# Performance work log

Hardware: AMD Instinct MI355X
Metric: run time of the kernel (lower is better)

The kernel has to match this reference:

```python
import jax, jax.numpy as jnp
import numpy as np

D_MODEL = 1024
N_HEADS = 16


def setup_inputs() -> dict:
    key0 = jax.random.key(0)
    ks = jax.random.split(key0, 13)
    B, Lq, Lk, D = 2, 1024, 2048, D_MODEL
    scale = 0.02
    inp = {
        "query": jax.random.normal(ks[0], (B, Lq, D), jnp.float32),
        "key": jax.random.normal(ks[1], (B, Lk, D), jnp.float32),
        "value": jax.random.normal(ks[2], (B, Lk, D), jnp.float32),
        "mask": jax.random.randint(ks[3], (B, 1, Lq, Lk), 0, 2, jnp.int32),
        "attn_bias": jax.random.normal(ks[4], (B, N_HEADS, Lq, Lk), jnp.float32) * 0.1,
        "Wq": jax.random.normal(ks[5], (D, D), jnp.float32) * scale,
        "bq": jnp.zeros((D,), jnp.float32),
        "Wk": jax.random.normal(ks[6], (D, D), jnp.float32) * scale,
        "bk": jnp.zeros((D,), jnp.float32),
        "Wv": jax.random.normal(ks[7], (D, D), jnp.float32) * scale,
        "bv": jnp.zeros((D,), jnp.float32),
        "Wo": jax.random.normal(ks[8], (D, D), jnp.float32) * scale,
        "bo": jnp.zeros((D,), jnp.float32),
    }
    return inp


def reference(query, key, value, mask, attn_bias, Wq, bq, Wk, bk, Wv, bv, Wo, bo):
    B, Lq, D = query.shape
    Lk = key.shape[1]
    H = N_HEADS
    dh = D // H
    # projections (torch Linear: x @ W.T + b), then split heads -> [B,H,L,dh]
    Q = (query @ Wq.T + bq).reshape(B, Lq, H, dh).transpose(0, 2, 1, 3)
    K = (key @ Wk.T + bk).reshape(B, Lk, H, dh).transpose(0, 2, 1, 3)
    V = (value @ Wv.T + bv).reshape(B, Lk, H, dh).transpose(0, 2, 1, 3)
    scores = jnp.einsum("bhqd,bhkd->bhqk", Q, K) / jnp.sqrt(jnp.float32(dh))
    scores = scores + attn_bias
    scores = jnp.where(mask == 0, jnp.float32(-1e9), scores)
    attn = jax.nn.softmax(scores, axis=-1)  # dropout disabled (eval / p=0)
    out = jnp.einsum("bhqk,bhkd->bhqd", attn, V)
    out = out.transpose(0, 2, 1, 3).reshape(B, Lq, D)
    out = out @ Wo.T + bo
    return out, attn
```

## Files before the change

kernel.cpp:

```cpp
#include <hip/hip_runtime.h>
#include <hip/hip_bf16.h>

typedef __hip_bfloat16 bf16;
typedef __bf16  bf16x8 __attribute__((ext_vector_type(8)));
typedef float   f32x4  __attribute__((ext_vector_type(4)));

static constexpr int DMODEL = 1024;
static constexpr int NHEADS = 16;
static constexpr int DHEAD  = 64;
static constexpr int BATCH  = 2;
static constexpr int SLQ    = 1024;
static constexpr int SLK    = 2048;
static constexpr size_t OUTQ = (size_t)BATCH * SLQ * DMODEL;

__device__ __forceinline__ void stage8(unsigned short* dst, const bf16* src) {
    *(int4*)dst = *(const int4*)src;
}
__device__ __forceinline__ void stage8(unsigned short* dst, const float* src) {
    const float4 a = *(const float4*)(src);
    const float4 b = *(const float4*)(src + 4);
    bf16 h[8];
    h[0] = __float2bfloat16(a.x); h[1] = __float2bfloat16(a.y);
    h[2] = __float2bfloat16(a.z); h[3] = __float2bfloat16(a.w);
    h[4] = __float2bfloat16(b.x); h[5] = __float2bfloat16(b.y);
    h[6] = __float2bfloat16(b.z); h[7] = __float2bfloat16(b.w);
    *(int4*)dst = *(const int4*)h;
}

__device__ __forceinline__ void store_one(bf16* p, float v) { *p = __float2bfloat16(v); }
__device__ __forceinline__ void store_one(float* p, float v) { *p = v; }

template <typename TA, typename TB>
__device__ __forceinline__ void gemm_core(const TA* __restrict__ At, int lda,
                                          const TB* __restrict__ Bt, int ldb,
                                          int K, f32x4 acc[2][2])
{
    __shared__ __align__(16) unsigned short As[64][40];
    __shared__ __align__(16) unsigned short Bs[64][40];
    const int tid  = threadIdx.x;
    const int lane = tid & 63;
    const int wave = tid >> 6;
    const int wr   = (wave >> 1) * 32;
    const int wc   = (wave & 1) * 32;
    const int lrow = lane & 15;
    const int koff = (lane >> 4) * 8;
    const int srow   = tid >> 2;
    const int schunk = (tid & 3) * 8;

    for (int kt = 0; kt < K; kt += 32) {
        stage8(&As[srow][schunk], At + (size_t)srow * lda + kt + schunk);
        stage8(&Bs[srow][schunk], Bt + (size_t)srow * ldb + kt + schunk);
        __syncthreads();
        bf16x8 a0 = *(const bf16x8*)(&As[wr      + lrow][koff]);
        bf16x8 a1 = *(const bf16x8*)(&As[wr + 16 + lrow][koff]);
        bf16x8 b0 = *(const bf16x8*)(&Bs[wc      + lrow][koff]);
        bf16x8 b1 = *(const bf16x8*)(&Bs[wc + 16 + lrow][koff]);
        acc[0][0] = __builtin_amdgcn_mfma_f32_16x16x32_bf16(a0, b0, acc[0][0], 0, 0, 0);
        acc[0][1] = __builtin_amdgcn_mfma_f32_16x16x32_bf16(a0, b1, acc[0][1], 0, 0, 0);
        acc[1][0] = __builtin_amdgcn_mfma_f32_16x16x32_bf16(a1, b0, acc[1][0], 0, 0, 0);
        acc[1][1] = __builtin_amdgcn_mfma_f32_16x16x32_bf16(a1, b1, acc[1][1], 0, 0, 0);
        __syncthreads();
    }
}

template <typename TA, typename TC>
__global__ __launch_bounds__(256)
void k_proj(const TA* __restrict__ A, const float* __restrict__ W,
            const float* __restrict__ bias, TC* __restrict__ C, int K, int N)
{
    const int m0 = blockIdx.x * 64;
    const int n0 = blockIdx.y * 64;
    f32x4 z = {0.f, 0.f, 0.f, 0.f};
    f32x4 acc[2][2] = {{z, z}, {z, z}};
    gemm_core(A + (size_t)m0 * K, K, W + (size_t)n0 * K, K, K, acc);
    const int lane = threadIdx.x & 63;
    const int wave = threadIdx.x >> 6;
    const int wr = (wave >> 1) * 32, wc = (wave & 1) * 32;
#pragma unroll
    for (int i = 0; i < 2; ++i)
#pragma unroll
        for (int j = 0; j < 2; ++j) {
            const int col = n0 + wc + j * 16 + (lane & 15);
            const float bv = bias[col];
#pragma unroll
            for (int r = 0; r < 4; ++r) {
                const int row = m0 + wr + i * 16 + (lane >> 4) * 4 + r;
                store_one(&C[(size_t)row * N + col], acc[i][j][r] + bv);
            }
        }
}

__global__ __launch_bounds__(256)
void k_projV(const float* __restrict__ A, const float* __restrict__ W,
             const float* __restrict__ bias, bf16* __restrict__ Vt)
{
    const int m0 = blockIdx.x * 64;
    const int n0 = blockIdx.y * 64;
    f32x4 z = {0.f, 0.f, 0.f, 0.f};
    f32x4 acc[2][2] = {{z, z}, {z, z}};
    gemm_core(A + (size_t)m0 * DMODEL, DMODEL, W + (size_t)n0 * DMODEL, DMODEL, DMODEL, acc);
    const int lane = threadIdx.x & 63;
    const int wave = threadIdx.x >> 6;
    const int wr = (wave >> 1) * 32, wc = (wave & 1) * 32;
#pragma unroll
    for (int i = 0; i < 2; ++i)
#pragma unroll
        for (int j = 0; j < 2; ++j) {
            const int col = n0 + wc + j * 16 + (lane & 15);
            const float bv = bias[col];
            const int h = col >> 6, d = col & 63;
            const int mb = m0 + wr + i * 16 + (lane >> 4) * 4;
            const int b = mb >> 11;
            const int kk = mb & 2047;
            bf16* dst = Vt + ((size_t)(b * NHEADS + h) * DHEAD + d) * SLK + kk;
#pragma unroll
            for (int r = 0; r < 4; ++r)
                dst[r] = __float2bfloat16(acc[i][j][r] + bv);
        }
}

__global__ __launch_bounds__(1024, 4)
void k_attn(const bf16* __restrict__ Qp, const bf16* __restrict__ Kp,
            const float* __restrict__ bias, const int* __restrict__ mask,
            const bf16* __restrict__ Vt, float* __restrict__ attn,
            bf16* __restrict__ ctx)
{
    constexpr int SST = 2052;
    constexpr int PST = 520;

    __shared__ __align__(16) float S[16 * SST];
    __shared__ __align__(16) bf16  Pc[16 * PST];
    __shared__ float m_s[16], inv_s[16];

    const int qt = blockIdx.x, bh = blockIdx.y;
    const int b = bh >> 4, h = bh & 15;
    const int q0 = qt * 16;
    const int tid  = threadIdx.x;
    const int lane = tid & 63, w = tid >> 6;
    const int lr = lane & 15, lk = lane >> 4;

    const bf16* qb = Qp + ((size_t)(b * SLQ + q0 + lr)) * DMODEL + h * DHEAD + lk * 8;
    const bf16x8 a0 = *(const bf16x8*)qb;
    const bf16x8 a1 = *(const bf16x8*)(qb + 32);

    const bf16* kb = Kp + (size_t)b * SLK * DMODEL + h * DHEAD + lk * 8;
#pragma unroll 2
    for (int ct = 0; ct < 8; ++ct) {
        const int c0 = w * 128 + ct * 16;
        const bf16* kp = kb + (size_t)(c0 + lr) * DMODEL;
        bf16x8 b0 = *(const bf16x8*)kp;
        bf16x8 b1 = *(const bf16x8*)(kp + 32);
        f32x4 acc = {0.f, 0.f, 0.f, 0.f};
        acc = __builtin_amdgcn_mfma_f32_16x16x32_bf16(a0, b0, acc, 0, 0, 0);
        acc = __builtin_amdgcn_mfma_f32_16x16x32_bf16(a1, b1, acc, 0, 0, 0);
#pragma unroll
        for (int r = 0; r < 4; ++r)
            S[(lk * 4 + r) * SST + c0 + lr] = acc[r] * 0.125f;
    }
    __syncthreads();

    {
        float* sp = &S[w * SST];
        const size_t brow = ((size_t)bh * SLQ + q0 + w) * SLK;
        const size_t mrow = ((size_t)b  * SLQ + q0 + w) * SLK;
        float mx = -3.0e38f;
#pragma unroll 2
        for (int j = 0; j < 8; ++j) {
            const int col = j * 256 + lane * 4;
            f32x4 v = *(const f32x4*)(sp + col);
            const float4 bb = *(const float4*)(bias + brow + col);
            const int4  mm = *(const int4*)(mask + mrow + col);
            float s0 = (mm.x == 0) ? -1e9f : v[0] + bb.x;
            float s1 = (mm.y == 0) ? -1e9f : v[1] + bb.y;
            float s2 = (mm.z == 0) ? -1e9f : v[2] + bb.z;
            float s3 = (mm.w == 0) ? -1e9f : v[3] + bb.w;
            f32x4 wv = {s0, s1, s2, s3};
            *(f32x4*)(sp + col) = wv;
            mx = fmaxf(mx, fmaxf(fmaxf(s0, s1), fmaxf(s2, s3)));
        }
#pragma unroll
        for (int d = 1; d < 64; d <<= 1) mx = fmaxf(mx, __shfl_xor(mx, d));
        float l = 0.f;
#pragma unroll 2
        for (int j = 0; j < 8; ++j) {
            const int col = j * 256 + lane * 4;
            const f32x4 v = *(const f32x4*)(sp + col);
            l += __expf(v[0] - mx) + __expf(v[1] - mx)
               + __expf(v[2] - mx) + __expf(v[3] - mx);
        }
#pragma unroll
        for (int d = 1; d < 64; d <<= 1) l += __shfl_xor(l, d);
        if (lane == 0) { m_s[w] = mx; inv_s[w] = 1.0f / l; }
    }
    __syncthreads();

    f32x4 pv = {0.f, 0.f, 0.f, 0.f};
    const int g = w >> 2, dg = w & 3;
    const bf16* vb = Vt + (size_t)bh * DHEAD * SLK + (size_t)(dg * 16 + lr) * SLK + lk * 8;
    for (int c = 0; c < 4; ++c) {
        const int ck0 = c * 512;
        {
            const int scol = lane * 8;
            const float m = m_s[w], inv = inv_s[w];
            const f32x4 s0 = *(const f32x4*)&S[w * SST + ck0 + scol];
            const f32x4 s1 = *(const f32x4*)&S[w * SST + ck0 + scol + 4];
            const f32x4 p0 = {__expf(s0[0] - m) * inv, __expf(s0[1] - m) * inv,
                              __expf(s0[2] - m) * inv, __expf(s0[3] - m) * inv};
            const f32x4 p1 = {__expf(s1[0] - m) * inv, __expf(s1[1] - m) * inv,
                              __expf(s1[2] - m) * inv, __expf(s1[3] - m) * inv};
            float* ap = attn + ((size_t)bh * SLQ + q0 + w) * SLK + ck0 + scol;
            __builtin_nontemporal_store(p0, (f32x4*)ap);
            __builtin_nontemporal_store(p1, (f32x4*)(ap + 4));
            bf16 t8[8] = {__float2bfloat16(p0[0]), __float2bfloat16(p0[1]),
                          __float2bfloat16(p0[2]), __float2bfloat16(p0[3]),
                          __float2bfloat16(p1[0]), __float2bfloat16(p1[1]),
                          __float2bfloat16(p1[2]), __float2bfloat16(p1[3])};
            *(int4*)&Pc[w * PST + scol] = *(const int4*)t8;
        }
        __syncthreads();
        const bf16* vc = vb + ck0;
#pragma unroll
        for (int i = 0; i < 4; ++i) {
            const int koff = (g * 4 + i) * 32;
            bf16x8 pa = *(const bf16x8*)&Pc[lr * PST + koff + lk * 8];
            bf16x8 vv = *(const bf16x8*)(vc + koff);
            pv = __builtin_amdgcn_mfma_f32_16x16x32_bf16(pa, vv, pv, 0, 0, 0);
        }
        __syncthreads();
    }

    float* rbuf = S;
    *(f32x4*)&rbuf[(w * 64 + lane) * 4] = pv;
    __syncthreads();
    if (g == 0) {
        f32x4 t = {0.f, 0.f, 0.f, 0.f};
#pragma unroll
        for (int gg = 0; gg < 4; ++gg)
            t += *(const f32x4*)&rbuf[((gg * 4 + dg) * 64 + lane) * 4];
        const int d = dg * 16 + lr;
#pragma unroll
        for (int r = 0; r < 4; ++r) {
            const int q = lk * 4 + r;
            ctx[((size_t)(b * SLQ + q0 + q)) * DMODEL + h * DHEAD + d] =
                __float2bfloat16(t[r]);
        }
    }
}

extern "C" void kernel_launch(void* const* d_in, const int* in_sizes, int n_in,
                              void* d_out, int out_size, void* d_ws, size_t ws_size,
                              hipStream_t stream)
{
    const float* query = (const float*)d_in[0];
    const float* key   = (const float*)d_in[1];
    const float* value = (const float*)d_in[2];
    const int*   mask  = (const int*)d_in[3];
    const float* bias  = (const float*)d_in[4];
    const float* Wq = (const float*)d_in[5];
    const float* bq = (const float*)d_in[6];
    const float* Wk = (const float*)d_in[7];
    const float* bk = (const float*)d_in[8];
    const float* Wv = (const float*)d_in[9];
    const float* bv = (const float*)d_in[10];
    const float* Wo = (const float*)d_in[11];
    const float* bo = (const float*)d_in[12];

    float* out  = (float*)d_out;
    float* attn = out + OUTQ;

    bf16* Qp  = (bf16*)d_ws;
    bf16* ctx = (bf16*)d_ws;
    bf16* Kp  = (bf16*)d_out;
    bf16* Vt  = (bf16*)d_ws + (size_t)4 * 1024 * 1024;

    dim3 blk(256);

    k_proj<float, bf16><<<dim3(BATCH * SLQ / 64, DMODEL / 64), blk, 0, stream>>>(query, Wq, bq, Qp, DMODEL, DMODEL);
    k_proj<float, bf16><<<dim3(BATCH * SLK / 64, DMODEL / 64), blk, 0, stream>>>(key,   Wk, bk, Kp, DMODEL, DMODEL);
    k_projV<<<dim3(BATCH * SLK / 64, DMODEL / 64), blk, 0, stream>>>(value, Wv, bv, Vt);
    k_attn<<<dim3(SLQ / 16, BATCH * NHEADS), dim3(1024), 0, stream>>>(Qp, Kp, bias, mask, Vt, attn, ctx);
    k_proj<bf16, float><<<dim3(BATCH * SLQ / 64, DMODEL / 64), blk, 0, stream>>>(ctx, Wo, bo, out, DMODEL, DMODEL);
}
```

Baseline: 740.4 us.

## Pre-convert inputs to bf16, fuse QKV projections into one 128x128-tile GEMM launch

Adds a single conversion kernel that casts the activations and weights to bf16 into scratch space inside the attn output buffer. Q/K/V projections are merged into one launch with 128x128 tiles and 4x4 MFMA per wave, and the output projection uses the same larger tile. This is meant to raise arithmetic intensity and stop converting fp32 inside the GEMM inner loop, at the cost of an extra full-memory pass for conversion and fewer blocks per launch.

```diff
diff --git a/kernel.cpp b/kernel.cpp
--- a/kernel.cpp
+++ b/kernel.cpp
@@ -13,109 +13,152 @@
 static constexpr int SLK    = 2048;
 static constexpr size_t OUTQ = (size_t)BATCH * SLQ * DMODEL;
 
-__device__ __forceinline__ void stage8(unsigned short* dst, const bf16* src) {
-    *(int4*)dst = *(const int4*)src;
-}
-__device__ __forceinline__ void stage8(unsigned short* dst, const float* src) {
-    const float4 a = *(const float4*)(src);
-    const float4 b = *(const float4*)(src + 4);
-    bf16 h[8];
-    h[0] = __float2bfloat16(a.x); h[1] = __float2bfloat16(a.y);
-    h[2] = __float2bfloat16(a.z); h[3] = __float2bfloat16(a.w);
-    h[4] = __float2bfloat16(b.x); h[5] = __float2bfloat16(b.y);
-    h[6] = __float2bfloat16(b.z); h[7] = __float2bfloat16(b.w);
-    *(int4*)dst = *(const int4*)h;
-}
-
-__device__ __forceinline__ void store_one(bf16* p, float v) { *p = __float2bfloat16(v); }
-__device__ __forceinline__ void store_one(float* p, float v) { *p = v; }
-
-template <typename TA, typename TB>
-__device__ __forceinline__ void gemm_core(const TA* __restrict__ At, int lda,
-                                          const TB* __restrict__ Bt, int ldb,
-                                          int K, f32x4 acc[2][2])
-{
-    __shared__ __align__(16) unsigned short As[64][40];
-    __shared__ __align__(16) unsigned short Bs[64][40];
+__global__ __launch_bounds__(256)
+void k_cvt(const float* __restrict__ q,  const float* __restrict__ k,
+           const float* __restrict__ v,  const float* __restrict__ wq,
+           const float* __restrict__ wk, const float* __restrict__ wv,
+           const float* __restrict__ wo,
+           bf16* __restrict__ qb,  bf16* __restrict__ kb,  bf16* __restrict__ vb,
+           bf16* __restrict__ wqb, bf16* __restrict__ wkb, bf16* __restrict__ wvb,
+           bf16* __restrict__ wob)
+{
+    const int seg = blockIdx.y;
+    const float* s; bf16* d; int n;
+    switch (seg) {
+        case 0:  s = q;  d = qb;  n = 2 * 1024 * 1024; break;
+        case 1:  s = k;  d = kb;  n = 4 * 1024 * 1024; break;
+        case 2:  s = v;  d = vb;  n = 4 * 1024 * 1024; break;
+        case 3:  s = wq; d = wqb; n = 1024 * 1024; break;
+        case 4:  s = wk; d = wkb; n = 1024 * 1024; break;
+        case 5:  s = wv; d = wvb; n = 1024 * 1024; break;
+        default: s = wo; d = wob; n = 1024 * 1024; break;
+    }
+    const int stride = gridDim.x * blockDim.x;
+    for (int i = blockIdx.x * blockDim.x + threadIdx.x; i * 8 < n; i += stride) {
+        const float4 a = *(const float4*)(s + (size_t)i * 8);
+        const float4 b = *(const float4*)(s + (size_t)i * 8 + 4);
+        bf16 h[8] = {__float2bfloat16(a.x), __float2bfloat16(a.y),
+                     __float2bfloat16(a.z), __float2bfloat16(a.w),
+                     __float2bfloat16(b.x), __float2bfloat16(b.y),
+                     __float2bfloat16(b.z), __float2bfloat16(b.w)};
+        *(int4*)(d + (size_t)i * 8) = *(const int4*)h;
+    }
+}
+
+__device__ __forceinline__ void gemm128(const bf16* __restrict__ A,
+                                        const bf16* __restrict__ W,
+                                        int m0, int n0, f32x4 acc[4][4])
+{
+    __shared__ __align__(16) unsigned short As[128][40];
+    __shared__ __align__(16) unsigned short Bs[128][40];
     const int tid  = threadIdx.x;
-    const int lane = tid & 63;
-    const int wave = tid >> 6;
-    const int wr   = (wave >> 1) * 32;
-    const int wc   = (wave & 1) * 32;
-    const int lrow = lane & 15;
-    const int koff = (lane >> 4) * 8;
-    const int srow   = tid >> 2;
-    const int schunk = (tid & 3) * 8;
-
-    for (int kt = 0; kt < K; kt += 32) {
-        stage8(&As[srow][schunk], At + (size_t)srow * lda + kt + schunk);
-        stage8(&Bs[srow][schunk], Bt + (size_t)srow * ldb + kt + schunk);
+    const int lane = tid & 63, w = tid >> 6;
+    const int wr = (w >> 1) * 64, wc = (w & 1) * 64;
+    const int lr = lane & 15, lk = lane >> 4;
+    const int srow = tid >> 1;
+    const int scol = (tid & 1) * 16;
+
+    const bf16* Ap = A + (size_t)(m0 + srow) * DMODEL + scol;
+    const bf16* Wp = W + (size_t)(n0 + srow) * DMODEL + scol;
+
+    for (int kt = 0; kt < DMODEL; kt += 32) {
+        *(int4*)&As[srow][scol]     = *(const int4*)(Ap + kt);
+        *(int4*)&As[srow][scol + 8] = *(const int4*)(Ap + kt + 8);
+        *(int4*)&Bs[srow][scol]     = *(const int4*)(Wp + kt);
+        *(int4*)&Bs[srow][scol + 8] = *(const int4*)(Wp + kt + 8);
         __syncthreads();
-        bf16x8 a0 = *(const bf16x8*)(&As[wr      + lrow][koff]);
-        bf16x8 a1 = *(const bf16x8*)(&As[wr + 16 + lrow][koff]);
-        bf16x8 b0 = *(const bf16x8*)(&Bs[wc      + lrow][koff]);
-        bf16x8 b1 = *(const bf16x8*)(&Bs[wc + 16 + lrow][koff]);
-        acc[0][0] = __builtin_amdgcn_mfma_f32_16x16x32_bf16(a0, b0, acc[0][0], 0, 0, 0);
-        acc[0][1] = __builtin_amdgcn_mfma_f32_16x16x32_bf16(a0, b1, acc[0][1], 0, 0, 0);
-        acc[1][0] = __builtin_amdgcn_mfma_f32_16x16x32_bf16(a1, b0, acc[1][0], 0, 0, 0);
-        acc[1][1] = __builtin_amdgcn_mfma_f32_16x16x32_bf16(a1, b1, acc[1][1], 0, 0, 0);
+        bf16x8 av[4], wv[4];
+#pragma unroll
+        for (int i = 0; i < 4; ++i)
+            av[i] = *(const bf16x8*)&As[wr + i * 16 + lr][lk * 8];
+#pragma unroll
+        for (int j = 0; j < 4; ++j)
+            wv[j] = *(const bf16x8*)&Bs[wc + j * 16 + lr][lk * 8];
+#pragma unroll
+        for (int i = 0; i < 4; ++i)
+#pragma unroll
+            for (int j = 0; j < 4; ++j)
+                acc[i][j] = __builtin_amdgcn_mfma_f32_16x16x32_bf16(av[i], wv[j], acc[i][j], 0, 0, 0);
         __syncthreads();
     }
 }
 
-template <typename TA, typename TC>
 __global__ __launch_bounds__(256)
-void k_proj(const TA* __restrict__ A, const float* __restrict__ W,
-            const float* __restrict__ bias, TC* __restrict__ C, int K, int N)
-{
-    const int m0 = blockIdx.x * 64;
-    const int n0 = blockIdx.y * 64;
-    f32x4 z = {0.f, 0.f, 0.f, 0.f};
-    f32x4 acc[2][2] = {{z, z}, {z, z}};
-    gemm_core(A + (size_t)m0 * K, K, W + (size_t)n0 * K, K, K, acc);
-    const int lane = threadIdx.x & 63;
-    const int wave = threadIdx.x >> 6;
-    const int wr = (wave >> 1) * 32, wc = (wave & 1) * 32;
-#pragma unroll
-    for (int i = 0; i < 2; ++i)
-#pragma unroll
-        for (int j = 0; j < 2; ++j) {
-            const int col = n0 + wc + j * 16 + (lane & 15);
-            const float bv = bias[col];
+void k_qkv(const bf16* __restrict__ qb, const bf16* __restrict__ kb,
+           const bf16* __restrict__ vb2,
+           const bf16* __restrict__ wqb, const bf16* __restrict__ wkb,
+           const bf16* __restrict__ wvb,
+           const float* __restrict__ bq, const float* __restrict__ bk,
+           const float* __restrict__ bvv,
+           bf16* __restrict__ Qp, bf16* __restrict__ Kp, bf16* __restrict__ Vt)
+{
+    const int which = blockIdx.z;
+    const int m0 = blockIdx.x * 128, n0 = blockIdx.y * 128;
+    if (which == 0 && m0 >= BATCH * SLQ) return;
+    const bf16* A = which == 0 ? qb : which == 1 ? kb : vb2;
+    const bf16* W = which == 0 ? wqb : which == 1 ? wkb : wvb;
+    const float* bias = which == 0 ? bq : which == 1 ? bk : bvv;
+
+    f32x4 acc[4][4] = {};
+    gemm128(A, W, m0, n0, acc);
+
+    const int tid = threadIdx.x, lane = tid & 63, w = tid >> 6;
+    const int wr = (w >> 1) * 64, wc = (w & 1) * 64;
+    const int lr = lane & 15, lk = lane >> 4;
+
+    if (which < 2) {
+        bf16* C = which == 0 ? Qp : Kp;
+#pragma unroll
+        for (int i = 0; i < 4; ++i)
+#pragma unroll
+            for (int j = 0; j < 4; ++j) {
+                const int col = n0 + wc + j * 16 + lr;
+                const float bvx = bias[col];
+#pragma unroll
+                for (int r = 0; r < 4; ++r) {
+                    const int row = m0 + wr + i * 16 + lk * 4 + r;
+                    C[(size_t)row * DMODEL + col] = __float2bfloat16(acc[i][j][r] + bvx);
+                }
+            }
+    } else {
+#pragma unroll
+        for (int i = 0; i < 4; ++i)
+#pragma unroll
+            for (int j = 0; j < 4; ++j) {
+                const int col = n0 + wc + j * 16 + lr;
+                const float bvx = bias[col];
+                const int h = col >> 6, d = col & 63;
+                const int mb = m0 + wr + i * 16 + lk * 4;
+                const int b = mb >> 11, kk = mb & 2047;
+                bf16* dst = Vt + ((size_t)(b * NHEADS + h) * DHEAD + d) * SLK + kk;
+#pragma unroll
+                for (int r = 0; r < 4; ++r)
+                    dst[r] = __float2bfloat16(acc[i][j][r] + bvx);
+            }
+    }
+}
+
+__global__ __launch_bounds__(256)
+void k_projO(const bf16* __restrict__ ctx, const bf16* __restrict__ wob,
+             const float* __restrict__ bo, float* __restrict__ out)
+{
+    const int m0 = blockIdx.x * 128, n0 = blockIdx.y * 128;
+    f32x4 acc[4][4] = {};
+    gemm128(ctx, wob, m0, n0, acc);
+    const int tid = threadIdx.x, lane = tid & 63, w = tid >> 6;
+    const int wr = (w >> 1) * 64, wc = (w & 1) * 64;
+    const int lr = lane & 15, lk = lane >> 4;
+#pragma unroll
+    for (int i = 0; i < 4; ++i)
+#pragma unroll
+        for (int j = 0; j < 4; ++j) {
+            const int col = n0 + wc + j * 16 + lr;
+            const float bvx = bo[col];
 #pragma unroll
             for (int r = 0; r < 4; ++r) {
-                const int row = m0 + wr + i * 16 + (lane >> 4) * 4 + r;
-                store_one(&C[(size_t)row * N + col], acc[i][j][r] + bv);
+                const int row = m0 + wr + i * 16 + lk * 4 + r;
+                out[(size_t)row * DMODEL + col] = acc[i][j][r] + bvx;
             }
-        }
-}
-
-__global__ __launch_bounds__(256)
-void k_projV(const float* __restrict__ A, const float* __restrict__ W,
-             const float* __restrict__ bias, bf16* __restrict__ Vt)
-{
-    const int m0 = blockIdx.x * 64;
-    const int n0 = blockIdx.y * 64;
-    f32x4 z = {0.f, 0.f, 0.f, 0.f};
-    f32x4 acc[2][2] = {{z, z}, {z, z}};
-    gemm_core(A + (size_t)m0 * DMODEL, DMODEL, W + (size_t)n0 * DMODEL, DMODEL, DMODEL, acc);
-    const int lane = threadIdx.x & 63;
-    const int wave = threadIdx.x >> 6;
-    const int wr = (wave >> 1) * 32, wc = (wave & 1) * 32;
-#pragma unroll
-    for (int i = 0; i < 2; ++i)
-#pragma unroll
-        for (int j = 0; j < 2; ++j) {
-            const int col = n0 + wc + j * 16 + (lane & 15);
-            const float bv = bias[col];
-            const int h = col >> 6, d = col & 63;
-            const int mb = m0 + wr + i * 16 + (lane >> 4) * 4;
-            const int b = mb >> 11;
-            const int kk = mb & 2047;
-            bf16* dst = Vt + ((size_t)(b * NHEADS + h) * DHEAD + d) * SLK + kk;
-#pragma unroll
-            for (int r = 0; r < 4; ++r)
-                dst[r] = __float2bfloat16(acc[i][j][r] + bv);
         }
 }
 
@@ -269,15 +312,22 @@
     float* attn = out + OUTQ;
 
     bf16* Qp  = (bf16*)d_ws;
-    bf16* ctx = (bf16*)d_ws;
+    bf16* ctx = Qp;
+    bf16* Wob = Qp + (size_t)2 * 1024 * 1024;
+    bf16* Vt  = Qp + (size_t)4 * 1024 * 1024;
     bf16* Kp  = (bf16*)d_out;
-    bf16* Vt  = (bf16*)d_ws + (size_t)4 * 1024 * 1024;
-
-    dim3 blk(256);
-
-    k_proj<float, bf16><<<dim3(BATCH * SLQ / 64, DMODEL / 64), blk, 0, stream>>>(query, Wq, bq, Qp, DMODEL, DMODEL);
-    k_proj<float, bf16><<<dim3(BATCH * SLK / 64, DMODEL / 64), blk, 0, stream>>>(key,   Wk, bk, Kp, DMODEL, DMODEL);
-    k_projV<<<dim3(BATCH * SLK / 64, DMODEL / 64), blk, 0, stream>>>(value, Wv, bv, Vt);
+
+    bf16* qbf = (bf16*)attn;
+    bf16* kbf = qbf + (size_t)2 * 1024 * 1024;
+    bf16* vbf = kbf + (size_t)4 * 1024 * 1024;
+    bf16* Wqb = vbf + (size_t)4 * 1024 * 1024;
+    bf16* Wkb = Wqb + (size_t)1024 * 1024;
+    bf16* Wvb = Wkb + (size_t)1024 * 1024;
+
+    k_cvt<<<dim3(256, 7), dim3(256), 0, stream>>>(query, key, value, Wq, Wk, Wv, Wo,
+                                                  qbf, kbf, vbf, Wqb, Wkb, Wvb, Wob);
+    k_qkv<<<dim3(32, 8, 3), dim3(256), 0, stream>>>(qbf, kbf, vbf, Wqb, Wkb, Wvb,
+                                                    bq, bk, bv, Qp, Kp, Vt);
     k_attn<<<dim3(SLQ / 16, BATCH * NHEADS), dim3(1024), 0, stream>>>(Qp, Kp, bias, mask, Vt, attn, ctx);
-    k_proj<bf16, float><<<dim3(BATCH * SLQ / 64, DMODEL / 64), blk, 0, stream>>>(ctx, Wo, bo, out, DMODEL, DMODEL);
-}
+    k_projO<<<dim3(16, 8), dim3(256), 0, stream>>>(ctx, Wob, bo, out);
+}
```

Measured after the change: 708.2 us. -4.3%, faster.
